# Optimization experiments

Measured on AMD Instinct MI355X. Metric: run time of the kernel, lower is better.

## Reference

```python
import jax, jax.numpy as jnp
import numpy as np

N_NODES = 50000
N_EDGES = 800000
DIM = 128
N_LAYERS = 5


def setup_inputs() -> dict:
    key = jax.random.key(0)
    k1, k2, k3, k4 = jax.random.split(key, 4)
    x = jax.random.normal(k1, (N_NODES, DIM), dtype=jnp.float32)
    edge_index = jax.random.randint(k2, (2, N_EDGES), 0, N_NODES, dtype=jnp.int64)
    # He-ish scale for stacked GCN layers so activations stay sane
    weights = jax.random.normal(k3, (N_LAYERS, DIM, DIM), dtype=jnp.float32) / jnp.sqrt(jnp.float32(DIM))
    biases = jax.random.normal(k4, (N_LAYERS, DIM), dtype=jnp.float32) * 0.01
    return {"x": x, "edge_index": edge_index, "weights": weights, "biases": biases}


def reference(x, edge_index, weights, biases):
    """5x (GCNConv -> ReLU). GCNConv: out = D^-1/2 (A+I) D^-1/2 (x W) + b."""
    n = x.shape[0]
    src, dst = edge_index[0], edge_index[1]
    # add self-loops (PyG GCNConv default)
    loop = jnp.arange(n, dtype=src.dtype)
    src_f = jnp.concatenate([src, loop])
    dst_f = jnp.concatenate([dst, loop])
    # symmetric normalization based on in-degree (incl. self loops)
    deg = jax.ops.segment_sum(jnp.ones(src_f.shape[0], dtype=x.dtype), dst_f, num_segments=n)
    dinv = jnp.where(deg > 0, jax.lax.rsqrt(deg), 0.0)
    norm = dinv[src_f] * dinv[dst_f]  # [E+N]

    for l in range(weights.shape[0]):
        h = x @ weights[l]                      # [N, D] dense transform
        msg = h[src_f] * norm[:, None]          # gather + scale  [E+N, D]
        x = jax.ops.segment_sum(msg, dst_f, num_segments=n) + biases[l]
        x = jax.nn.relu(x)
    return x
```

## Files before the change

kernel.cpp:

```cpp
#include <hip/hip_runtime.h>
#include <hip/hip_bf16.h>
#include <hip/hip_fp16.h>


#define GCN_DIM 128

typedef short bf16x8 __attribute__((ext_vector_type(8)));
typedef float f32x4 __attribute__((ext_vector_type(4)));
typedef unsigned int u32x4 __attribute__((ext_vector_type(4)));

__device__ __forceinline__ unsigned short f2bf(float f) {
    unsigned int u = __float_as_uint(f);
    u += 0x7FFFu + ((u >> 16) & 1u);
    return (unsigned short)(u >> 16);
}
__device__ __forceinline__ float bf2f(unsigned short b) {
    return __uint_as_float(((unsigned int)b) << 16);
}
__device__ __forceinline__ float bflo(unsigned int p) { return __uint_as_float(p << 16); }
__device__ __forceinline__ float bfhi(unsigned int p) { return __uint_as_float(p & 0xFFFF0000u); }

__global__ void count_kernel(const int* __restrict__ dst, int* __restrict__ cnt,
                             int* __restrict__ rank, int E) {
    int e = blockIdx.x * 256 + threadIdx.x;
    if (e < E) rank[e] = atomicAdd(&cnt[dst[e]], 1);
}

__global__ __launch_bounds__(256) void scan_part_kernel(const int* __restrict__ cnt,
                                                        int* __restrict__ loc,
                                                        int* __restrict__ bsum, int n) {
    __shared__ int s[256];
    int t = threadIdx.x;
    int i0 = blockIdx.x * 1024 + t * 4;
    int v0 = (i0 + 0 < n) ? cnt[i0 + 0] : 0;
    int v1 = (i0 + 1 < n) ? cnt[i0 + 1] : 0;
    int v2 = (i0 + 2 < n) ? cnt[i0 + 2] : 0;
    int v3 = (i0 + 3 < n) ? cnt[i0 + 3] : 0;
    int tsum = v0 + v1 + v2 + v3;
    s[t] = tsum;
    __syncthreads();
    for (int d = 1; d < 256; d <<= 1) {
        int u = (t >= d) ? s[t - d] : 0;
        __syncthreads();
        s[t] += u;
        __syncthreads();
    }
    int base = s[t] - tsum;
    if (i0 + 0 < n) loc[i0 + 0] = base; base += v0;
    if (i0 + 1 < n) loc[i0 + 1] = base; base += v1;
    if (i0 + 2 < n) loc[i0 + 2] = base; base += v2;
    if (i0 + 3 < n) loc[i0 + 3] = base;
    if (t == 255) bsum[blockIdx.x] = s[255];
}

__global__ __launch_bounds__(256) void scan_top_kernel(int* __restrict__ bsum, int nb) {
    __shared__ int s[256];
    int t = threadIdx.x;
    int v = (t < nb) ? bsum[t] : 0;
    s[t] = v;
    __syncthreads();
    for (int d = 1; d < 256; d <<= 1) {
        int u = (t >= d) ? s[t - d] : 0;
        __syncthreads();
        s[t] += u;
        __syncthreads();
    }
    if (t < nb) bsum[t] = s[t] - v;
}

__global__ void scan_add_kernel(int* __restrict__ offs,
                                const int* __restrict__ bsum, const int* __restrict__ cnt,
                                float* __restrict__ dinv, int n, int E) {
    int i = blockIdx.x * 256 + threadIdx.x;
    if (i < n) {
        offs[i] = offs[i] + bsum[i >> 10];
        dinv[i] = rsqrtf((float)cnt[i] + 1.0f);
    }
    if (i == 0) offs[n] = E;
}

__global__ void fill_kernel(const int* __restrict__ src, const int* __restrict__ dst,
                            const int* __restrict__ rank, const int* __restrict__ offs,
                            unsigned int* __restrict__ edat, int E) {
    int e = blockIdx.x * 256 + threadIdx.x;
    if (e < E) {
        int d = dst[e];
        int p = offs[d] + rank[e];
        edat[p] = ((unsigned int)src[e]) << 5;
    }
}

__global__ void split_x_kernel(const float* __restrict__ x, unsigned short* __restrict__ xh,
                               unsigned short* __restrict__ xl, int total) {
    int i = (blockIdx.x * 256 + threadIdx.x) * 4;
    if (i >= total) return;
    float4 v = *(const float4*)&x[i];
    ushort4 h4, l4;
    h4.x = f2bf(v.x); l4.x = f2bf(v.x - bf2f(h4.x));
    h4.y = f2bf(v.y); l4.y = f2bf(v.y - bf2f(h4.y));
    h4.z = f2bf(v.z); l4.z = f2bf(v.z - bf2f(h4.z));
    h4.w = f2bf(v.w); l4.w = f2bf(v.w - bf2f(h4.w));
    *(ushort4*)&xh[i] = h4;
    *(ushort4*)&xl[i] = l4;
}

__global__ void wsplit_kernel(const float* __restrict__ Wall, unsigned short* __restrict__ Wfh,
                              unsigned short* __restrict__ Wfl, int total) {
    int idx = blockIdx.x * 256 + threadIdx.x;
    if (idx >= total) return;
    int l = idx >> 14;
    int rem = idx & 16383;
    int k = rem >> 7;
    int nn = rem & 127;
    float v = Wall[idx];
    unsigned short hi = f2bf(v);
    unsigned short lo = f2bf(v - bf2f(hi));
    int t = nn >> 4, ln = nn & 15;
    int ks = k >> 5, q = (k >> 3) & 3, j = k & 7;
    int o = ((((l << 5) | (t << 2) | ks) << 6) | (q << 4) | ln) * 8 + j;
    Wfh[o] = hi;
    Wfl[o] = lo;
}

__global__ __launch_bounds__(256) void gemm_mfma_kernel(
    const unsigned short* __restrict__ xh, const unsigned short* __restrict__ xl,
    const unsigned short* __restrict__ Wfh, const unsigned short* __restrict__ Wfl,
    const float* __restrict__ dinv,
    unsigned short* __restrict__ h, int n) {
    __shared__ unsigned short ldsW[2][8192];
    int tid = threadIdx.x;
    int wave = tid >> 6, lane = tid & 63;
    int q = lane >> 4, ln = lane & 15;
    int rowbase = blockIdx.x * 64 + wave * 16;
    bf16x8 A[4][2];
    {
        int ar = rowbase + ln;
        if (ar >= n) ar = n - 1;
        size_t base = (size_t)ar * GCN_DIM;
#pragma unroll
        for (int ks = 0; ks < 4; ks++) {
            A[ks][0] = *(const bf16x8*)&xh[base + ks * 32 + q * 8];
            A[ks][1] = *(const bf16x8*)&xl[base + ks * 32 + q * 8];
        }
    }
    int node = rowbase + ln;
    float di = (node < n) ? dinv[node] : 0.f;
#pragma unroll
    for (int half = 0; half < 2; half++) {
        if (half) __syncthreads();
        {
            const uint4* gh = (const uint4*)(Wfh + half * 8192);
            const uint4* gl = (const uint4*)(Wfl + half * 8192);
            uint4* sh = (uint4*)ldsW[0];
            uint4* sl = (uint4*)ldsW[1];
#pragma unroll
            for (int r = 0; r < 4; r++) {
                sh[tid + 256 * r] = gh[tid + 256 * r];
                sl[tid + 256 * r] = gl[tid + 256 * r];
            }
        }
        __syncthreads();
#pragma unroll
        for (int tp = 0; tp < 2; tp++) {
            int tta = tp * 2, ttb = tp * 2 + 1;
            f32x4 accA = (f32x4)(0.f), accB = (f32x4)(0.f);
#pragma unroll
            for (int ks = 0; ks < 4; ks++) {
                int foA = ((tta * 4 + ks) * 64 + lane) * 8;
                int foB = ((ttb * 4 + ks) * 64 + lane) * 8;
                bf16x8 bhA = *(const bf16x8*)&ldsW[0][foA];
                bf16x8 blA = *(const bf16x8*)&ldsW[1][foA];
                bf16x8 bhB = *(const bf16x8*)&ldsW[0][foB];
                bf16x8 blB = *(const bf16x8*)&ldsW[1][foB];
                accA = __builtin_amdgcn_mfma_f32_16x16x32_bf16(bhA, A[ks][0], accA, 0, 0, 0);
                accB = __builtin_amdgcn_mfma_f32_16x16x32_bf16(bhB, A[ks][0], accB, 0, 0, 0);
                accA = __builtin_amdgcn_mfma_f32_16x16x32_bf16(bhA, A[ks][1], accA, 0, 0, 0);
                accB = __builtin_amdgcn_mfma_f32_16x16x32_bf16(bhB, A[ks][1], accB, 0, 0, 0);
                accA = __builtin_amdgcn_mfma_f32_16x16x32_bf16(blA, A[ks][0], accA, 0, 0, 0);
                accB = __builtin_amdgcn_mfma_f32_16x16x32_bf16(blB, A[ks][0], accB, 0, 0, 0);
            }
            if (node < n) {
                int ta = half * 4 + tta, tb = half * 4 + ttb;
                ushort4 oA, oB;
                oA.x = f2bf(accA[0] * di); oA.y = f2bf(accA[1] * di);
                oA.z = f2bf(accA[2] * di); oA.w = f2bf(accA[3] * di);
                oB.x = f2bf(accB[0] * di); oB.y = f2bf(accB[1] * di);
                oB.z = f2bf(accB[2] * di); oB.w = f2bf(accB[3] * di);
                *(ushort4*)&h[((size_t)ta * n + node) * 16 + q * 4] = oA;
                *(ushort4*)&h[((size_t)tb * n + node) * 16 + q * 4] = oB;
            }
        }
    }
}

__global__ __launch_bounds__(256) void agg_kernel(
    const unsigned short* __restrict__ h,
    const unsigned int* __restrict__ edat,
    const int* __restrict__ offs,
    const float* __restrict__ dinv, const float* __restrict__ bias,
    unsigned short* __restrict__ xh_out,
    unsigned short* __restrict__ xl_out,
    float* __restrict__ fout, int n) {
    int tid = threadIdx.x;
    int wave = tid >> 6, lane = tid & 63;
    int sub = lane >> 3, ln = lane & 7;
    int p  = ln & 1;
    int s4 = ln >> 1;
    int slice = blockIdx.x & 7;
    int node = (blockIdx.x >> 3) * 32 + wave * 8 + sub;
    if (node >= n) return;
    const char* hs = (const char*)h + (size_t)slice * n * 32;
    unsigned int p16 = (unsigned int)(p << 4);
    float di = dinv[node];
    float a0 = 0.f, a1 = 0.f, a2 = 0.f, a3 = 0.f;
    float a4 = 0.f, a5 = 0.f, a6 = 0.f, a7 = 0.f;
#define ACC8(g) do { \
        a0 += bflo((g).x); a1 += bfhi((g).x); \
        a2 += bflo((g).y); a3 += bfhi((g).y); \
        a4 += bflo((g).z); a5 += bfhi((g).z); \
        a6 += bflo((g).w); a7 += bfhi((g).w); } while (0)
    int s = offs[node], e = offs[node + 1];
    int j = s;
    for (; j + 8 <= e; j += 8) {
        uint2 od = *(const uint2*)&edat[j + (s4 << 1)];
        uint4 g0 = *(const uint4*)(hs + (od.x + p16));
        uint4 g1 = *(const uint4*)(hs + (od.y + p16));
        __builtin_amdgcn_sched_barrier(0);
        ACC8(g0);
        ACC8(g1);
    }
    if (j + 4 <= e) {
        unsigned int od = edat[j + s4];
        uint4 g0 = *(const uint4*)(hs + (od + p16));
        ACC8(g0);
        j += 4;
    }
    int rem = e - j;
    if (s4 < rem) {
        unsigned int od = edat[j + s4];
        uint4 g0 = *(const uint4*)(hs + (od + p16));
        ACC8(g0);
    }
    a0 += __shfl_xor(a0, 2); a0 += __shfl_xor(a0, 4);
    a1 += __shfl_xor(a1, 2); a1 += __shfl_xor(a1, 4);
    a2 += __shfl_xor(a2, 2); a2 += __shfl_xor(a2, 4);
    a3 += __shfl_xor(a3, 2); a3 += __shfl_xor(a3, 4);
    a4 += __shfl_xor(a4, 2); a4 += __shfl_xor(a4, 4);
    a5 += __shfl_xor(a5, 2); a5 += __shfl_xor(a5, 4);
    a6 += __shfl_xor(a6, 2); a6 += __shfl_xor(a6, 4);
    a7 += __shfl_xor(a7, 2); a7 += __shfl_xor(a7, 4);
    {
        uint4 sp4 = *(const uint4*)(hs + ((unsigned int)node * 32u + p16));
        ACC8(sp4);
    }
#undef ACC8
    if (s4 == 0) {
        int cg = slice * 16 + p * 8;
        float4 b0 = *(const float4*)&bias[cg];
        float4 b1 = *(const float4*)&bias[cg + 4];
        float r0 = fmaxf(fmaf(di, a0, b0.x), 0.f);
        float r1 = fmaxf(fmaf(di, a1, b0.y), 0.f);
        float r2 = fmaxf(fmaf(di, a2, b0.z), 0.f);
        float r3 = fmaxf(fmaf(di, a3, b0.w), 0.f);
        float r4 = fmaxf(fmaf(di, a4, b1.x), 0.f);
        float r5 = fmaxf(fmaf(di, a5, b1.y), 0.f);
        float r6 = fmaxf(fmaf(di, a6, b1.z), 0.f);
        float r7 = fmaxf(fmaf(di, a7, b1.w), 0.f);
        if (fout) {
            f32x4 o0 = {r0, r1, r2, r3};
            f32x4 o1 = {r4, r5, r6, r7};
            float* fp = &fout[(size_t)node * GCN_DIM + cg];
            __builtin_nontemporal_store(o0, (f32x4*)fp);
            __builtin_nontemporal_store(o1, (f32x4*)(fp + 4));
        } else {
            unsigned short h0 = f2bf(r0), h1 = f2bf(r1), h2 = f2bf(r2), h3 = f2bf(r3);
            unsigned short h4 = f2bf(r4), h5 = f2bf(r5), h6 = f2bf(r6), h7 = f2bf(r7);
            u32x4 hp = {(unsigned int)h0 | ((unsigned int)h1 << 16),
                        (unsigned int)h2 | ((unsigned int)h3 << 16),
                        (unsigned int)h4 | ((unsigned int)h5 << 16),
                        (unsigned int)h6 | ((unsigned int)h7 << 16)};
            unsigned short l0 = f2bf(r0 - bf2f(h0)), l1 = f2bf(r1 - bf2f(h1));
            unsigned short l2 = f2bf(r2 - bf2f(h2)), l3 = f2bf(r3 - bf2f(h3));
            unsigned short l4 = f2bf(r4 - bf2f(h4)), l5 = f2bf(r5 - bf2f(h5));
            unsigned short l6 = f2bf(r6 - bf2f(h6)), l7 = f2bf(r7 - bf2f(h7));
            u32x4 lp = {(unsigned int)l0 | ((unsigned int)l1 << 16),
                        (unsigned int)l2 | ((unsigned int)l3 << 16),
                        (unsigned int)l4 | ((unsigned int)l5 << 16),
                        (unsigned int)l6 | ((unsigned int)l7 << 16)};
            __builtin_nontemporal_store(hp, (u32x4*)&xh_out[(size_t)node * GCN_DIM + cg]);
            __builtin_nontemporal_store(lp, (u32x4*)&xl_out[(size_t)node * GCN_DIM + cg]);
        }
    }
}

extern "C" void kernel_launch(void* const* d_in, const int* in_sizes, int n_in,
                              void* d_out, int out_size, void* d_ws, size_t ws_size,
                              hipStream_t stream) {
    const float* x0    = (const float*)d_in[0];
    const int*   edges = (const int*)d_in[1];
    const float* Wall  = (const float*)d_in[2];
    const float* Ball  = (const float*)d_in[3];
    float* out = (float*)d_out;

    const int n = in_sizes[0] / GCN_DIM;
    const int E = in_sizes[1] / 2;
    const int L = in_sizes[2] / (GCN_DIM * GCN_DIM);

    int*   cnt    = (int*)d_ws;
    float* dinv   = (float*)(cnt + n);
    int*   offs   = (int*)(dinv + n);
    int*   bsum   = offs + n + 16;
    int*   rank   = bsum + 64;
    unsigned int* edat = (unsigned int*)(rank + E);
    unsigned short* h   = (unsigned short*)(edat + E);
    unsigned short* xh  = h  + (size_t)n * GCN_DIM;
    unsigned short* xl  = xh + (size_t)n * GCN_DIM;
    unsigned short* Wfh = xl + (size_t)n * GCN_DIM;
    unsigned short* Wfl = Wfh + (size_t)L * GCN_DIM * GCN_DIM;

    const int* src = edges;
    const int* dst = edges + E;

    int nb_n = (n + 255) / 256;
    int nb_e = (E + 255) / 256;
    int nb_scan = (n + 1023) / 1024;

    hipMemsetAsync(cnt, 0, (size_t)n * sizeof(int), stream);
    count_kernel<<<nb_e, 256, 0, stream>>>(dst, cnt, rank, E);
    scan_part_kernel<<<nb_scan, 256, 0, stream>>>(cnt, offs, bsum, n);
    scan_top_kernel<<<1, 256, 0, stream>>>(bsum, nb_scan);
    scan_add_kernel<<<nb_n, 256, 0, stream>>>(offs, bsum, cnt, dinv, n, E);
    fill_kernel<<<nb_e, 256, 0, stream>>>(src, dst, rank, offs, edat, E);

    int xtotal = n * GCN_DIM;
    split_x_kernel<<<(xtotal / 4 + 255) / 256, 256, 0, stream>>>(x0, xh, xl, xtotal);
    int wtotal = L * GCN_DIM * GCN_DIM;
    wsplit_kernel<<<(wtotal + 255) / 256, 256, 0, stream>>>(Wall, Wfh, Wfl, wtotal);

    int gemm_blocks = (n + 63) / 64;
    int agg_blocks  = ((n + 31) / 32) * 8;

    for (int l = 0; l < L; l++) {
        gemm_mfma_kernel<<<gemm_blocks, 256, 0, stream>>>(
            xh, xl, Wfh + (size_t)l * GCN_DIM * GCN_DIM, Wfl + (size_t)l * GCN_DIM * GCN_DIM,
            dinv, h, n);
        agg_kernel<<<agg_blocks, 256, 0, stream>>>(
            h, edat, offs, dinv, Ball + (size_t)l * GCN_DIM,
            xh, xl, (l == L - 1) ? out : nullptr, n);
    }
}
```

Baseline: 413.6 us.

## Widen h feature slices to 32 columns, halving aggregation block passes

The intermediate h layout changes from 8 slices of 16 bf16 columns (32 bytes per node) to 4 slices of 32 columns (64 bytes per node). The GEMM epilogue, the edge-index pre-shift and the aggregation kernel are all updated to match. The aggregation kernel now uses 4 lanes per 64-byte row and 2 edge groups per node, and loads four edge indices per step with nontemporal loads. This halves how often each edge list is re-read across slices and makes each gather 64 bytes contiguous, at the cost of fewer independent gathers in flight per lane group and a reworked tail.

```diff
diff --git a/kernel.cpp b/kernel.cpp
--- a/kernel.cpp
+++ b/kernel.cpp
@@ -86,7 +86,7 @@
     if (e < E) {
         int d = dst[e];
         int p = offs[d] + rank[e];
-        edat[p] = ((unsigned int)src[e]) << 5;
+        edat[p] = ((unsigned int)src[e]) << 6;
     }
 }
 
@@ -180,14 +180,16 @@
                 accB = __builtin_amdgcn_mfma_f32_16x16x32_bf16(blB, A[ks][0], accB, 0, 0, 0);
             }
             if (node < n) {
-                int ta = half * 4 + tta, tb = half * 4 + ttb;
+                int ta = half * 4 + tta;
+                int slice2 = ta >> 1;
+                size_t sb = ((size_t)slice2 * n + node) * 32 + q * 4;
                 ushort4 oA, oB;
                 oA.x = f2bf(accA[0] * di); oA.y = f2bf(accA[1] * di);
                 oA.z = f2bf(accA[2] * di); oA.w = f2bf(accA[3] * di);
                 oB.x = f2bf(accB[0] * di); oB.y = f2bf(accB[1] * di);
                 oB.z = f2bf(accB[2] * di); oB.w = f2bf(accB[3] * di);
-                *(ushort4*)&h[((size_t)ta * n + node) * 16 + q * 4] = oA;
-                *(ushort4*)&h[((size_t)tb * n + node) * 16 + q * 4] = oB;
+                *(ushort4*)&h[sb] = oA;
+                *(ushort4*)&h[sb + 16] = oB;
             }
         }
     }
@@ -204,12 +206,12 @@
     int tid = threadIdx.x;
     int wave = tid >> 6, lane = tid & 63;
     int sub = lane >> 3, ln = lane & 7;
-    int p  = ln & 1;
-    int s4 = ln >> 1;
-    int slice = blockIdx.x & 7;
-    int node = (blockIdx.x >> 3) * 32 + wave * 8 + sub;
+    int p  = ln & 3;
+    int s2 = ln >> 2;
+    int slice = blockIdx.x & 3;
+    int node = (blockIdx.x >> 2) * 32 + wave * 8 + sub;
     if (node >= n) return;
-    const char* hs = (const char*)h + (size_t)slice * n * 32;
+    const char* hs = (const char*)h + (size_t)slice * n * 64;
     unsigned int p16 = (unsigned int)(p << 4);
     float di = dinv[node];
     float a0 = 0.f, a1 = 0.f, a2 = 0.f, a3 = 0.f;
@@ -222,40 +224,51 @@
     int s = offs[node], e = offs[node + 1];
     int j = s;
     for (; j + 8 <= e; j += 8) {
-        uint2 od = *(const uint2*)&edat[j + (s4 << 1)];
+        u32x4 od = __builtin_nontemporal_load((const u32x4*)&edat[j + (s2 << 2)]);
         uint4 g0 = *(const uint4*)(hs + (od.x + p16));
         uint4 g1 = *(const uint4*)(hs + (od.y + p16));
+        uint4 g2 = *(const uint4*)(hs + (od.z + p16));
+        uint4 g3 = *(const uint4*)(hs + (od.w + p16));
         __builtin_amdgcn_sched_barrier(0);
         ACC8(g0);
         ACC8(g1);
+        ACC8(g2);
+        ACC8(g3);
     }
     if (j + 4 <= e) {
-        unsigned int od = edat[j + s4];
+        uint2 od = *(const uint2*)&edat[j + (s2 << 1)];
+        uint4 g0 = *(const uint4*)(hs + (od.x + p16));
+        uint4 g1 = *(const uint4*)(hs + (od.y + p16));
+        ACC8(g0);
+        ACC8(g1);
+        j += 4;
+    }
+    if (j + 2 <= e) {
+        unsigned int od = edat[j + s2];
         uint4 g0 = *(const uint4*)(hs + (od + p16));
         ACC8(g0);
-        j += 4;
-    }
-    int rem = e - j;
-    if (s4 < rem) {
-        unsigned int od = edat[j + s4];
+        j += 2;
+    }
+    if (s2 == 0 && j < e) {
+        unsigned int od = edat[j];
         uint4 g0 = *(const uint4*)(hs + (od + p16));
         ACC8(g0);
     }
-    a0 += __shfl_xor(a0, 2); a0 += __shfl_xor(a0, 4);
-    a1 += __shfl_xor(a1, 2); a1 += __shfl_xor(a1, 4);
-    a2 += __shfl_xor(a2, 2); a2 += __shfl_xor(a2, 4);
-    a3 += __shfl_xor(a3, 2); a3 += __shfl_xor(a3, 4);
-    a4 += __shfl_xor(a4, 2); a4 += __shfl_xor(a4, 4);
-    a5 += __shfl_xor(a5, 2); a5 += __shfl_xor(a5, 4);
-    a6 += __shfl_xor(a6, 2); a6 += __shfl_xor(a6, 4);
-    a7 += __shfl_xor(a7, 2); a7 += __shfl_xor(a7, 4);
+    a0 += __shfl_xor(a0, 4);
+    a1 += __shfl_xor(a1, 4);
+    a2 += __shfl_xor(a2, 4);
+    a3 += __shfl_xor(a3, 4);
+    a4 += __shfl_xor(a4, 4);
+    a5 += __shfl_xor(a5, 4);
+    a6 += __shfl_xor(a6, 4);
+    a7 += __shfl_xor(a7, 4);
     {
-        uint4 sp4 = *(const uint4*)(hs + ((unsigned int)node * 32u + p16));
+        uint4 sp4 = *(const uint4*)(hs + ((unsigned int)node * 64u + p16));
         ACC8(sp4);
     }
 #undef ACC8
-    if (s4 == 0) {
-        int cg = slice * 16 + p * 8;
+    if (s2 == 0) {
+        int cg = slice * 32 + p * 8;
         float4 b0 = *(const float4*)&bias[cg];
         float4 b1 = *(const float4*)&bias[cg + 4];
         float r0 = fmaxf(fmaf(di, a0, b0.x), 0.f);
@@ -338,7 +351,7 @@
     wsplit_kernel<<<(wtotal + 255) / 256, 256, 0, stream>>>(Wall, Wfh, Wfl, wtotal);
 
     int gemm_blocks = (n + 63) / 64;
-    int agg_blocks  = ((n + 31) / 32) * 8;
+    int agg_blocks  = ((n + 31) / 32) * 4;
 
     for (int l = 0; l < L; l++) {
         gemm_mfma_kernel<<<gemm_blocks, 256, 0, stream>>>(
```

After: 415.4 us. Within noise of the previous version (+0.4%).
